# Kernel tuning notes

Hardware: AMD Instinct MI355X
Metric: run time of the kernel (lower is better)

## Reference

```python
import jax, jax.numpy as jnp
import numpy as np

BS, M, N = 8, 64, 4096
K_SEL = 32
TEMP = 5.0  # temperature_update_tf(tempIncr=5, epoch=0, n_epochs=2) -> constant at step 0
EPS = 1e-20


def setup_inputs() -> dict:
    key = jax.random.key(0)
    k1, k2 = jax.random.split(key)
    logits = jax.random.normal(k1, (M, N), dtype=jnp.float32)
    u = jax.random.uniform(k2, (BS, M, N), dtype=jnp.float32)
    return {"logits": logits, "u": u}


def reference(logits, u):
    # Gumbel(0, 0.001) noise, exactly as in the TF code
    gn = -0.001 * jnp.log(-jnp.log(u + EPS) + EPS)          # (BS, M, N)
    perturbed = logits[None, :, :] + gn                      # (BS, M, N)
    # tf.nn.top_k(tf.nn.top_k(x, k).indices, k).values then reverse ==
    # top-k indices sorted ascending
    _, idx = jax.lax.top_k(perturbed, K_SEL)                 # (BS, M, k)
    idx_sorted = jnp.sort(idx, axis=-1)
    hard = jax.nn.one_hot(idx_sorted, N, dtype=logits.dtype)  # (BS, M, k, N)
    # exclusive cumsum over the k axis
    cum_mask = jnp.cumsum(hard, axis=-2) - hard               # (BS, M, k, N)
    # log(exp(logits) * (1 - cumMask + eps)) == logits + log(1 - cumMask + eps)
    scores = (logits[None, :, None, :]
              + jnp.log(1.0 - cum_mask + EPS)
              + gn[:, :, None, :]) / TEMP                     # (BS, M, k, N)
    soft = jax.nn.softmax(scores, axis=-1)
    # straight-through: hard forward, soft backward
    return jax.lax.stop_gradient(hard - soft) + soft
```

## Files before the change

kernel.cpp:

```cpp
#include <hip/hip_runtime.h>
#include <math.h>

#define BSZ 8
#define MROWS 64
#define NCOLS 4096
#define KSEL 32
#define EPSF 1e-20f
#define NEG_INF (-3.402823466e+38f)

__global__ __launch_bounds__(256) void topk_select_kernel(
    const float* __restrict__ logits,
    const float* __restrict__ u,
    int* __restrict__ idx_out)
{
    __shared__ float vals[NCOLS];

    const int r   = blockIdx.x;
    const int m   = r & (MROWS - 1);
    const int tid = threadIdx.x;

    const float4* u4 = (const float4*)(u + (size_t)r * NCOLS);
    const float4* l4 = (const float4*)(logits + (size_t)m * NCOLS);

    #pragma unroll
    for (int c = 0; c < 4; ++c) {
        int q = (c << 8) + tid;
        float4 uu = u4[q];
        float4 lg = l4[q];
        float px = lg.x - 0.001f * logf(-logf(uu.x + EPSF) + EPSF);
        float py = lg.y - 0.001f * logf(-logf(uu.y + EPSF) + EPSF);
        float pz = lg.z - 0.001f * logf(-logf(uu.z + EPSF) + EPSF);
        float pw = lg.w - 0.001f * logf(-logf(uu.w + EPSF) + EPSF);
        int col   = q << 2;
        int chunk = col >> 6;
        int base  = chunk << 6;
        vals[base + ((col + 0 + chunk) & 63)] = px;
        vals[base + ((col + 1 + chunk) & 63)] = py;
        vals[base + ((col + 2 + chunk) & 63)] = pz;
        vals[base + ((col + 3 + chunk) & 63)] = pw;
    }
    __syncthreads();

    if (tid >= 64) return;
    const int lane = tid;

    float lmax = NEG_INF;
    int   lidx = 0x7FFFFFFF;
    {
        const int cb = lane << 6;
        #pragma unroll 8
        for (int c = 0; c < 64; ++c) {
            float v = vals[cb + ((c + lane) & 63)];
            if (v > lmax) { lmax = v; lidx = cb + c; }
        }
    }

    unsigned long long removed = 0ull;
    int sel_reg = 0x7FFFFFFF;
    for (int it = 0; it < KSEL; ++it) {
        float bv = lmax; int bi = lidx;
        #pragma unroll
        for (int off = 32; off; off >>= 1) {
            float ov = __shfl_xor(bv, off);
            int   oi = __shfl_xor(bi, off);
            if (ov > bv || (ov == bv && oi < bi)) { bv = ov; bi = oi; }
        }
        if (lane == it) sel_reg = bi;

        const int wl = bi >> 6;
        if (lane == wl) removed |= (1ull << (bi & 63));

        unsigned long long rm = __shfl(removed, wl);
        float nv = vals[(wl << 6) + ((lane + wl) & 63)];
        int   ni = (wl << 6) + lane;
        if ((rm >> lane) & 1ull) nv = NEG_INF;
        #pragma unroll
        for (int off = 32; off; off >>= 1) {
            float ov = __shfl_xor(nv, off);
            int   oi = __shfl_xor(ni, off);
            if (ov > nv || (ov == nv && oi < ni)) { nv = ov; ni = oi; }
        }
        if (lane == wl) { lmax = nv; lidx = ni; }
    }

    int myw = sel_reg;
    int rank = 0;
    #pragma unroll
    for (int j = 0; j < KSEL; ++j) {
        int wj = __shfl(sel_reg, j);
        rank += (wj < myw) ? 1 : 0;
    }
    if (lane < KSEL) idx_out[r * KSEL + rank] = myw;
}

__global__ __launch_bounds__(256) void onehot_write_kernel(
    const int* __restrict__ idx,
    float* __restrict__ out)
{
    const int rho  = (blockIdx.x << 2) | (threadIdx.x >> 6);
    const int lane = threadIdx.x & 63;

    const int t  = idx[rho];
    const int tq = t >> 2;
    const int te = t & 3;

    float4* orow = (float4*)(out + (size_t)rho * NCOLS);
    #pragma unroll
    for (int c = 0; c < 16; ++c) {
        int q = (c << 6) + lane;
        bool hit = (q == tq);
        float4 z;
        z.x = (hit && te == 0) ? 1.0f : 0.0f;
        z.y = (hit && te == 1) ? 1.0f : 0.0f;
        z.z = (hit && te == 2) ? 1.0f : 0.0f;
        z.w = (hit && te == 3) ? 1.0f : 0.0f;
        orow[q] = z;
    }
}

extern "C" void kernel_launch(void* const* d_in, const int* in_sizes, int n_in,
                              void* d_out, int out_size, void* d_ws, size_t ws_size,
                              hipStream_t stream) {
    const float* logits = (const float*)d_in[0];
    const float* u      = (const float*)d_in[1];
    float* out          = (float*)d_out;
    int*   idx          = (int*)d_ws;

    topk_select_kernel<<<BSZ * MROWS, 256, 0, stream>>>(logits, u, idx);
    onehot_write_kernel<<<(BSZ * MROWS * KSEL) / 4, 256, 0, stream>>>(idx, out);
}
```

Baseline: 307.8 us.

## Fuse top-k selection and one-hot output into one kernel with idle-wave zero filling

Merges the selection and one-hot write kernels into a single launch. While wave 0 runs the serial top-k selection, the other three waves zero-fill output rows 5..31. Wave 0 then writes rows 0..4 with their one-hot values, and after a barrier the remaining ones are scattered into rows 5..31. This removes the second launch and the index round-trip through workspace, and hides the output write traffic behind the selection latency. In exchange the grid has only 512 blocks, each writing 512 KB, so store parallelism may be lower than with the separate write kernel.

```diff
diff --git a/kernel.cpp b/kernel.cpp
--- a/kernel.cpp
+++ b/kernel.cpp
@@ -8,12 +8,13 @@
 #define EPSF 1e-20f
 #define NEG_INF (-3.402823466e+38f)
 
-__global__ __launch_bounds__(256) void topk_select_kernel(
+__global__ __launch_bounds__(256) void topk_fused_kernel(
     const float* __restrict__ logits,
     const float* __restrict__ u,
-    int* __restrict__ idx_out)
+    float* __restrict__ out)
 {
     __shared__ float vals[NCOLS];
+    __shared__ int   si[KSEL];
 
     const int r   = blockIdx.x;
     const int m   = r & (MROWS - 1);
@@ -41,80 +42,88 @@
     }
     __syncthreads();
 
-    if (tid >= 64) return;
-    const int lane = tid;
+    const int lane = tid & 63;
+    const int w    = tid >> 6;
+    float* orow0   = out + (size_t)r * KSEL * NCOLS;
 
-    float lmax = NEG_INF;
-    int   lidx = 0x7FFFFFFF;
-    {
-        const int cb = lane << 6;
-        #pragma unroll 8
-        for (int c = 0; c < 64; ++c) {
-            float v = vals[cb + ((c + lane) & 63)];
-            if (v > lmax) { lmax = v; lidx = cb + c; }
+    if (w == 0) {
+        float lmax = NEG_INF;
+        int   lidx = 0x7FFFFFFF;
+        {
+            const int cb = lane << 6;
+            #pragma unroll 8
+            for (int c = 0; c < 64; ++c) {
+                float v = vals[cb + ((c + lane) & 63)];
+                if (v > lmax) { lmax = v; lidx = cb + c; }
+            }
+        }
+        unsigned long long removed = 0ull;
+        int sel_reg = 0x7FFFFFFF;
+        for (int it = 0; it < KSEL; ++it) {
+            float bv = lmax; int bi = lidx;
+            #pragma unroll
+            for (int off = 32; off; off >>= 1) {
+                float ov = __shfl_xor(bv, off);
+                int   oi = __shfl_xor(bi, off);
+                if (ov > bv || (ov == bv && oi < bi)) { bv = ov; bi = oi; }
+            }
+            if (lane == it) sel_reg = bi;
+
+            const int wl = bi >> 6;
+            if (lane == wl) removed |= (1ull << (bi & 63));
+
+            unsigned long long rm = __shfl(removed, wl);
+            float nv = vals[(wl << 6) + ((lane + wl) & 63)];
+            int   ni = (wl << 6) + lane;
+            if ((rm >> lane) & 1ull) nv = NEG_INF;
+            #pragma unroll
+            for (int off = 32; off; off >>= 1) {
+                float ov = __shfl_xor(nv, off);
+                int   oi = __shfl_xor(ni, off);
+                if (ov > nv || (ov == nv && oi < ni)) { nv = ov; ni = oi; }
+            }
+            if (lane == wl) { lmax = nv; lidx = ni; }
+        }
+        int myw = sel_reg;
+        int rank = 0;
+        #pragma unroll
+        for (int j = 0; j < KSEL; ++j) {
+            int wj = __shfl(sel_reg, j);
+            rank += (wj < myw) ? 1 : 0;
+        }
+        if (lane < KSEL) si[rank] = myw;
+
+        for (int j = 0; j < 5; ++j) {
+            int t  = si[j];
+            int tq = t >> 2;
+            int te = t & 3;
+            float4* orow = (float4*)(orow0 + (size_t)j * NCOLS);
+            #pragma unroll
+            for (int c = 0; c < 16; ++c) {
+                int q = (c << 6) + lane;
+                bool hit = (q == tq);
+                float4 z;
+                z.x = (hit && te == 0) ? 1.0f : 0.0f;
+                z.y = (hit && te == 1) ? 1.0f : 0.0f;
+                z.z = (hit && te == 2) ? 1.0f : 0.0f;
+                z.w = (hit && te == 3) ? 1.0f : 0.0f;
+                orow[q] = z;
+            }
+        }
+    } else {
+        const int start = 5 + (w - 1) * 9;
+        const float4 z4 = make_float4(0.f, 0.f, 0.f, 0.f);
+        for (int j = start; j < start + 9; ++j) {
+            float4* orow = (float4*)(orow0 + (size_t)j * NCOLS);
+            #pragma unroll
+            for (int c = 0; c < 16; ++c) orow[(c << 6) + lane] = z4;
         }
     }
 
-    unsigned long long removed = 0ull;
-    int sel_reg = 0x7FFFFFFF;
-    for (int it = 0; it < KSEL; ++it) {
-        float bv = lmax; int bi = lidx;
-        #pragma unroll
-        for (int off = 32; off; off >>= 1) {
-            float ov = __shfl_xor(bv, off);
-            int   oi = __shfl_xor(bi, off);
-            if (ov > bv || (ov == bv && oi < bi)) { bv = ov; bi = oi; }
-        }
-        if (lane == it) sel_reg = bi;
+    __syncthreads();
 
-        const int wl = bi >> 6;
-        if (lane == wl) removed |= (1ull << (bi & 63));
-
-        unsigned long long rm = __shfl(removed, wl);
-        float nv = vals[(wl << 6) + ((lane + wl) & 63)];
-        int   ni = (wl << 6) + lane;
-        if ((rm >> lane) & 1ull) nv = NEG_INF;
-        #pragma unroll
-        for (int off = 32; off; off >>= 1) {
-            float ov = __shfl_xor(nv, off);
-            int   oi = __shfl_xor(ni, off);
-            if (ov > nv || (ov == nv && oi < ni)) { nv = ov; ni = oi; }
-        }
-        if (lane == wl) { lmax = nv; lidx = ni; }
-    }
-
-    int myw = sel_reg;
-    int rank = 0;
-    #pragma unroll
-    for (int j = 0; j < KSEL; ++j) {
-        int wj = __shfl(sel_reg, j);
-        rank += (wj < myw) ? 1 : 0;
-    }
-    if (lane < KSEL) idx_out[r * KSEL + rank] = myw;
-}
-
-__global__ __launch_bounds__(256) void onehot_write_kernel(
-    const int* __restrict__ idx,
-    float* __restrict__ out)
-{
-    const int rho  = (blockIdx.x << 2) | (threadIdx.x >> 6);
-    const int lane = threadIdx.x & 63;
-
-    const int t  = idx[rho];
-    const int tq = t >> 2;
-    const int te = t & 3;
-
-    float4* orow = (float4*)(out + (size_t)rho * NCOLS);
-    #pragma unroll
-    for (int c = 0; c < 16; ++c) {
-        int q = (c << 6) + lane;
-        bool hit = (q == tq);
-        float4 z;
-        z.x = (hit && te == 0) ? 1.0f : 0.0f;
-        z.y = (hit && te == 1) ? 1.0f : 0.0f;
-        z.z = (hit && te == 2) ? 1.0f : 0.0f;
-        z.w = (hit && te == 3) ? 1.0f : 0.0f;
-        orow[q] = z;
+    if (tid >= 5 && tid < KSEL) {
+        orow0[(size_t)tid * NCOLS + (size_t)si[tid]] = 1.0f;
     }
 }
 
@@ -124,8 +133,6 @@
     const float* logits = (const float*)d_in[0];
     const float* u      = (const float*)d_in[1];
     float* out          = (float*)d_out;
-    int*   idx          = (int*)d_ws;
 
-    topk_select_kernel<<<BSZ * MROWS, 256, 0, stream>>>(logits, u, idx);
-    onehot_write_kernel<<<(BSZ * MROWS * KSEL) / 4, 256, 0, stream>>>(idx, out);
+    topk_fused_kernel<<<BSZ * MROWS, 256, 0, stream>>>(logits, u, out);
 }
```

Result: faster. 273.2 us (-11.3%).
